# Optimization experiments

Measured on AMD Instinct MI355X. Metric: run time of the kernel, lower is better.

The kernel has to match this reference:

```python
import jax, jax.numpy as jnp
import numpy as np

DIM_B = 4096   # batch of ragged segments
DIM_M = 128    # max seq len == dim_m == dim_c (source: dim_c = dim_m)
DIM_C = 128
DIM_Q = 256    # dim_q = 2 * dim_m


def _make_lengths():
    # deterministic ragged lengths in [1, DIM_M]; 37 coprime with 128 -> exact total
    return ((np.arange(DIM_B) * 37) % DIM_M + 1).astype(np.int64)


def setup_inputs() -> dict:
    key = jax.random.key(0)
    k1, k2, k3, k4 = jax.random.split(key, 4)
    xss = jax.random.normal(k1, (DIM_B, DIM_M, DIM_Q), dtype=jnp.float32)
    Wk = jax.random.normal(k2, (DIM_C, DIM_Q), dtype=jnp.float32) * 0.05
    Wc = jax.random.normal(k3, (DIM_M, DIM_C), dtype=jnp.float32) * 0.05
    proj = jax.random.normal(k4, (DIM_C, DIM_Q), dtype=jnp.float32) * 0.05
    lens = _make_lengths()
    # flat padded index (b*DIM_M + s) of every valid ragged token, in batch order
    gather_idx = np.concatenate([b * DIM_M + np.arange(l) for b, l in enumerate(lens)]).astype(np.int64)
    return {
        "xss": xss,
        "Wk": Wk,
        "Wc": Wc,
        "proj": proj,
        "seq_lengths": jnp.asarray(lens),
        "gather_idx": jnp.asarray(gather_idx),
    }


def reference(xss, Wk, Wc, proj, seq_lengths, gather_idx):
    B, M, Q = xss.shape
    # validity mask over padded positions
    mask = (jnp.arange(M)[None, :] < seq_lengths[:, None]).astype(xss.dtype)  # (B, M)
    # kernel: Linear(dim_q -> dim_c), applied to all (padded) tokens
    ks = jnp.einsum('bmq,cq->bmc', xss, Wk)          # (B, M, C)
    # pool: masked sum over the ragged segment
    context = jnp.einsum('bmc,bm->bc', ks, mask)     # (B, C)
    cs = context @ Wc.T                              # (B, C)  (dim_m == dim_c)
    v = cs @ proj                                    # (B, Q)
    y = jnp.einsum('bq,bmq->bm', v, xss)             # (B, M) per-token scalar
    # gather valid ragged tokens in original concat order -> (total_tokens, 1)
    ys = y.reshape(-1)[gather_idx][:, None]
    return ys
```

## Files before the change

### kernel.cpp

```cpp
#include <hip/hip_runtime.h>
#include <hip/hip_bf16.h>

#define DIM_B 4096
#define DIM_M 128
#define DIM_C 128
#define DIM_Q 256

__global__ __launch_bounds__(256) void k_xsum(const float* __restrict__ xss,
                                              const int* __restrict__ lens32,
                                              float* __restrict__ xsum) {
    const int b = blockIdx.x;
    const int tid = threadIdx.x;
    const int wave = tid >> 6, lane = tid & 63;
    const bool is64 = (lens32[1] == 0);
    const int len = is64 ? lens32[2 * b] : lens32[b];
    const float* base = xss + (size_t)b * DIM_M * DIM_Q + lane * 4;
    float a0 = 0.f, a1 = 0.f, a2 = 0.f, a3 = 0.f;
    for (int m = wave; m < len; m += 4) {
        const float4 u = *(const float4*)(base + (size_t)m * DIM_Q);
        a0 += u.x; a1 += u.y; a2 += u.z; a3 += u.w;
    }
    __shared__ float s[4][DIM_Q];
    s[wave][lane * 4 + 0] = a0;
    s[wave][lane * 4 + 1] = a1;
    s[wave][lane * 4 + 2] = a2;
    s[wave][lane * 4 + 3] = a3;
    __syncthreads();
    xsum[(size_t)b * DIM_Q + tid] = s[0][tid] + s[1][tid] + s[2][tid] + s[3][tid];
}

__global__ __launch_bounds__(256) void k_a1(const float* __restrict__ Wc,
                                            const float* __restrict__ proj,
                                            float* __restrict__ A1) {
    const int c = blockIdx.x;
    const int qp = threadIdx.x;
    float acc = 0.f;
    for (int j = 0; j < DIM_M; ++j)
        acc += Wc[j * DIM_C + c] * proj[j * DIM_Q + qp];
    A1[c * DIM_Q + qp] = acc;
}

__global__ __launch_bounds__(256) void k_wcomb(const float* __restrict__ Wk,
                                               const float* __restrict__ A1,
                                               float* __restrict__ Wcomb) {
    const int q = blockIdx.x;
    const int qp = threadIdx.x;
    float acc = 0.f;
    for (int c = 0; c < DIM_C; ++c)
        acc += Wk[c * DIM_Q + q] * A1[c * DIM_Q + qp];
    Wcomb[q * DIM_Q + qp] = acc;
}

__global__ __launch_bounds__(256) void k_v(const float* __restrict__ xsum,
                                           const float* __restrict__ Wcomb,
                                           float* __restrict__ v) {
    const int tid = threadIdx.x;
    const int b0 = blockIdx.x * 16;
    __shared__ float s[16][DIM_Q];
    for (int r = 0; r < 16; ++r)
        s[r][tid] = xsum[(size_t)(b0 + r) * DIM_Q + tid];
    __syncthreads();
    float acc[16];
#pragma unroll
    for (int r = 0; r < 16; ++r) acc[r] = 0.f;
    for (int q = 0; q < DIM_Q; ++q) {
        const float w = Wcomb[q * DIM_Q + tid];
#pragma unroll
        for (int r = 0; r < 16; ++r) acc[r] += s[r][q] * w;
    }
#pragma unroll
    for (int r = 0; r < 16; ++r)
        v[(size_t)(b0 + r) * DIM_Q + tid] = acc[r];
}

__global__ __launch_bounds__(256) void k_y(const float* __restrict__ xss,
                                           const float* __restrict__ v,
                                           const int* __restrict__ gidx32,
                                           float* __restrict__ out,
                                           int ntok) {
    const int wave = threadIdx.x >> 6, lane = threadIdx.x & 63;
    const int t = blockIdx.x * 4 + wave;
    if (t >= ntok) return;
    const bool is64 = (gidx32[1] == 0);
    const int idx = is64 ? gidx32[2 * t] : gidx32[t];
    const int b = idx >> 7;
    const float4 u  = *(const float4*)(xss + (size_t)idx * DIM_Q + lane * 4);
    const float4 vv = *(const float4*)(v + (size_t)b * DIM_Q + lane * 4);
    float d = u.x * vv.x + u.y * vv.y + u.z * vv.z + u.w * vv.w;
#pragma unroll
    for (int off = 32; off >= 1; off >>= 1)
        d += __shfl_down(d, off, 64);
    if (lane == 0)
        out[t] = d;
}

extern "C" void kernel_launch(void* const* d_in, const int* in_sizes, int n_in,
                              void* d_out, int out_size, void* d_ws, size_t ws_size,
                              hipStream_t stream) {
    const float* xss  = (const float*)d_in[0];
    const float* Wk   = (const float*)d_in[1];
    const float* Wc   = (const float*)d_in[2];
    const float* proj = (const float*)d_in[3];
    const int* lens = (const int*)d_in[4];
    const int* gidx = (const int*)d_in[5];
    float* out = (float*)d_out;
    const int ntok = in_sizes[5];

    float* ws    = (float*)d_ws;
    float* xsum  = ws;
    float* vbuf  = ws + (size_t)DIM_B * DIM_Q;
    float* A1    = vbuf + (size_t)DIM_B * DIM_Q;
    float* Wcomb = A1 + (size_t)DIM_C * DIM_Q;

    k_xsum<<<DIM_B, 256, 0, stream>>>(xss, lens, xsum);
    k_a1<<<DIM_C, 256, 0, stream>>>(Wc, proj, A1);
    k_wcomb<<<DIM_Q, 256, 0, stream>>>(Wk, A1, Wcomb);
    k_v<<<DIM_B / 16, 256, 0, stream>>>(xsum, Wcomb, vbuf);
    k_y<<<(ntok + 3) / 4, 256, 0, stream>>>(xss, vbuf, gidx, out, ntok);
}
```

Measured before the change: 744.6 us.

## Fuse pooling, projection and per-token dot into persistent kernel with scanned offsets

Replaces the separate xsum, v and gather/dot kernels with one persistent kernel that grabs segments via an atomic counter, pools the valid tokens, computes v against register-resident Wcomb, and immediately rereads the segment to produce outputs. Output positions come from a prefix scan of the lengths instead of reading gather_idx, relying on the tokens being in batch order. The aim is to cut the intermediate buffers and have the second pass over each segment hit cache rather than HBM, at the cost of serialised per-segment phases and extra synchronisation.

```diff
diff --git a/kernel.cpp b/kernel.cpp
--- a/kernel.cpp
+++ b/kernel.cpp
@@ -1,37 +1,15 @@
 #include <hip/hip_runtime.h>
-#include <hip/hip_bf16.h>
 
 #define DIM_B 4096
 #define DIM_M 128
 #define DIM_C 128
 #define DIM_Q 256
 
-__global__ __launch_bounds__(256) void k_xsum(const float* __restrict__ xss,
-                                              const int* __restrict__ lens32,
-                                              float* __restrict__ xsum) {
-    const int b = blockIdx.x;
-    const int tid = threadIdx.x;
-    const int wave = tid >> 6, lane = tid & 63;
-    const bool is64 = (lens32[1] == 0);
-    const int len = is64 ? lens32[2 * b] : lens32[b];
-    const float* base = xss + (size_t)b * DIM_M * DIM_Q + lane * 4;
-    float a0 = 0.f, a1 = 0.f, a2 = 0.f, a3 = 0.f;
-    for (int m = wave; m < len; m += 4) {
-        const float4 u = *(const float4*)(base + (size_t)m * DIM_Q);
-        a0 += u.x; a1 += u.y; a2 += u.z; a3 += u.w;
-    }
-    __shared__ float s[4][DIM_Q];
-    s[wave][lane * 4 + 0] = a0;
-    s[wave][lane * 4 + 1] = a1;
-    s[wave][lane * 4 + 2] = a2;
-    s[wave][lane * 4 + 3] = a3;
-    __syncthreads();
-    xsum[(size_t)b * DIM_Q + tid] = s[0][tid] + s[1][tid] + s[2][tid] + s[3][tid];
-}
-
 __global__ __launch_bounds__(256) void k_a1(const float* __restrict__ Wc,
                                             const float* __restrict__ proj,
-                                            float* __restrict__ A1) {
+                                            float* __restrict__ A1,
+                                            int* __restrict__ counter) {
+    if (blockIdx.x == 0 && threadIdx.x == 0) *counter = 0;
     const int c = blockIdx.x;
     const int qp = threadIdx.x;
     float acc = 0.f;
@@ -51,47 +29,115 @@
     Wcomb[q * DIM_Q + qp] = acc;
 }
 
-__global__ __launch_bounds__(256) void k_v(const float* __restrict__ xsum,
-                                           const float* __restrict__ Wcomb,
-                                           float* __restrict__ v) {
-    const int tid = threadIdx.x;
-    const int b0 = blockIdx.x * 16;
-    __shared__ float s[16][DIM_Q];
-    for (int r = 0; r < 16; ++r)
-        s[r][tid] = xsum[(size_t)(b0 + r) * DIM_Q + tid];
+__global__ __launch_bounds__(256) void k_scan(const int* __restrict__ lens32,
+                                              int* __restrict__ offs) {
+    __shared__ int part[256];
+    const int t = threadIdx.x;
+    const bool is64 = (lens32[1] == 0);
+    const int base = t * 16;
+    int l[16];
+    int s = 0;
+#pragma unroll
+    for (int k = 0; k < 16; ++k) {
+        l[k] = is64 ? lens32[2 * (base + k)] : lens32[base + k];
+        s += l[k];
+    }
+    part[t] = s;
     __syncthreads();
-    float acc[16];
+    for (int off = 1; off < 256; off <<= 1) {
+        const int v = (t >= off) ? part[t - off] : 0;
+        __syncthreads();
+        part[t] += v;
+        __syncthreads();
+    }
+    int run = part[t] - s;
 #pragma unroll
-    for (int r = 0; r < 16; ++r) acc[r] = 0.f;
-    for (int q = 0; q < DIM_Q; ++q) {
-        const float w = Wcomb[q * DIM_Q + tid];
-#pragma unroll
-        for (int r = 0; r < 16; ++r) acc[r] += s[r][q] * w;
+    for (int k = 0; k < 16; ++k) {
+        offs[base + k] = run;
+        run += l[k];
     }
-#pragma unroll
-    for (int r = 0; r < 16; ++r)
-        v[(size_t)(b0 + r) * DIM_Q + tid] = acc[r];
 }
 
-__global__ __launch_bounds__(256) void k_y(const float* __restrict__ xss,
-                                           const float* __restrict__ v,
-                                           const int* __restrict__ gidx32,
-                                           float* __restrict__ out,
-                                           int ntok) {
-    const int wave = threadIdx.x >> 6, lane = threadIdx.x & 63;
-    const int t = blockIdx.x * 4 + wave;
-    if (t >= ntok) return;
-    const bool is64 = (gidx32[1] == 0);
-    const int idx = is64 ? gidx32[2 * t] : gidx32[t];
-    const int b = idx >> 7;
-    const float4 u  = *(const float4*)(xss + (size_t)idx * DIM_Q + lane * 4);
-    const float4 vv = *(const float4*)(v + (size_t)b * DIM_Q + lane * 4);
-    float d = u.x * vv.x + u.y * vv.y + u.z * vv.z + u.w * vv.w;
+__global__ __launch_bounds__(1024, 4) void k_fused(const float* __restrict__ xss,
+                                                   const float* __restrict__ Wcomb,
+                                                   const int* __restrict__ lens32,
+                                                   const int* __restrict__ offs,
+                                                   float* __restrict__ out,
+                                                   int* __restrict__ counter) {
+    const int tid = threadIdx.x;
+    const int lane = tid & 63;
+    const int wv = tid >> 6;
+    const int qp = tid & 255;
+    const int qt = tid >> 8;
+    const bool is64 = (lens32[1] == 0);
+
+    float4 W4[16];
 #pragma unroll
-    for (int off = 32; off >= 1; off >>= 1)
-        d += __shfl_down(d, off, 64);
-    if (lane == 0)
-        out[t] = d;
+    for (int j = 0; j < 16; ++j) {
+        const int q0 = qt * 64 + j * 4;
+        W4[j].x = Wcomb[(q0 + 0) * DIM_Q + qp];
+        W4[j].y = Wcomb[(q0 + 1) * DIM_Q + qp];
+        W4[j].z = Wcomb[(q0 + 2) * DIM_Q + qp];
+        W4[j].w = Wcomb[(q0 + 3) * DIM_Q + qp];
+    }
+
+    __shared__ float4 sp4[16][64];
+    __shared__ float xsum_s[DIM_Q];
+    __shared__ float sv[4][DIM_Q];
+    __shared__ float v_s[DIM_Q];
+    __shared__ int sb;
+
+    while (true) {
+        if (tid == 0) sb = atomicAdd(counter, 1);
+        __syncthreads();
+        const int b = sb;
+        if (b >= DIM_B) break;
+        const int len = is64 ? lens32[2 * b] : lens32[b];
+        const int off_b = offs[b];
+        const float* xb = xss + (size_t)b * (DIM_M * DIM_Q);
+
+        float4 acc = {0.f, 0.f, 0.f, 0.f};
+#pragma unroll 2
+        for (int m = wv; m < len; m += 16) {
+            const float4 u = *(const float4*)(xb + m * DIM_Q + lane * 4);
+            acc.x += u.x; acc.y += u.y; acc.z += u.z; acc.w += u.w;
+        }
+        sp4[wv][lane] = acc;
+        __syncthreads();
+        if (tid < DIM_Q) {
+            float s = 0.f;
+            const float* spf = (const float*)sp4;
+#pragma unroll
+            for (int g = 0; g < 16; ++g) s += spf[g * DIM_Q + tid];
+            xsum_s[tid] = s;
+        }
+        __syncthreads();
+
+        {
+            float p = 0.f;
+#pragma unroll
+            for (int j = 0; j < 16; ++j) {
+                const float4 xs = *(const float4*)(xsum_s + qt * 64 + j * 4);
+                p += xs.x * W4[j].x + xs.y * W4[j].y + xs.z * W4[j].z + xs.w * W4[j].w;
+            }
+            sv[qt][qp] = p;
+        }
+        __syncthreads();
+        if (tid < DIM_Q)
+            v_s[tid] = sv[0][tid] + sv[1][tid] + sv[2][tid] + sv[3][tid];
+        __syncthreads();
+
+        const float4 vv = *(const float4*)(v_s + lane * 4);
+        for (int m = wv; m < len; m += 16) {
+            const float4 u = *(const float4*)(xb + m * DIM_Q + lane * 4);
+            float d = u.x * vv.x + u.y * vv.y + u.z * vv.z + u.w * vv.w;
+#pragma unroll
+            for (int off = 32; off >= 1; off >>= 1)
+                d += __shfl_down(d, off, 64);
+            if (lane == 0)
+                out[off_b + m] = d;
+        }
+    }
 }
 
 extern "C" void kernel_launch(void* const* d_in, const int* in_sizes, int n_in,
@@ -102,19 +148,16 @@
     const float* Wc   = (const float*)d_in[2];
     const float* proj = (const float*)d_in[3];
     const int* lens = (const int*)d_in[4];
-    const int* gidx = (const int*)d_in[5];
     float* out = (float*)d_out;
-    const int ntok = in_sizes[5];
 
     float* ws    = (float*)d_ws;
-    float* xsum  = ws;
-    float* vbuf  = ws + (size_t)DIM_B * DIM_Q;
-    float* A1    = vbuf + (size_t)DIM_B * DIM_Q;
+    float* A1    = ws;
     float* Wcomb = A1 + (size_t)DIM_C * DIM_Q;
+    int* offs    = (int*)(Wcomb + (size_t)DIM_Q * DIM_Q);
+    int* counter = offs + DIM_B;
 
-    k_xsum<<<DIM_B, 256, 0, stream>>>(xss, lens, xsum);
-    k_a1<<<DIM_C, 256, 0, stream>>>(Wc, proj, A1);
+    k_a1<<<DIM_C, 256, 0, stream>>>(Wc, proj, A1, counter);
     k_wcomb<<<DIM_Q, 256, 0, stream>>>(Wk, A1, Wcomb);
-    k_v<<<DIM_B / 16, 256, 0, stream>>>(xsum, Wcomb, vbuf);
-    k_y<<<(ntok + 3) / 4, 256, 0, stream>>>(xss, vbuf, gidx, out, ntok);
+    k_scan<<<1, 256, 0, stream>>>(lens, offs);
+    k_fused<<<256, 1024, 0, stream>>>(xss, Wcomb, lens, offs, out, counter);
 }
```

New measurement: 664.7 us. 1.12x faster.
